# Performance work log

Hardware: AMD Instinct MI355X
Metric: run time of the kernel (lower is better)

The kernel has to match this reference:

```python
import jax, jax.numpy as jnp
import numpy as np

TEMPERATURE = 0.5   # cfg.LOSS.TEMPERATURE
REG = 0.5           # Sinkhorn entropic regularization
NUM_ITER = 100      # numItermax in forward call
STOP_THR = 1e-9

BS, NUM_CLASSES, DIM = 16384, 1000, 512


def _l2norm(x):
    return x / jnp.linalg.norm(x, axis=-1, keepdims=True)


def setup_inputs() -> dict:
    key = jax.random.key(0)
    k1, k2, k3 = jax.random.split(key, 3)
    features = _l2norm(jax.random.normal(k1, (BS, DIM), jnp.float32))
    text_features = _l2norm(jax.random.normal(k2, (NUM_CLASSES, DIM), jnp.float32))
    ratios = jax.random.uniform(k3, (NUM_CLASSES,), jnp.float32)
    ratios = ratios / ratios.sum()  # class prior, sums to 1
    return {"features": features, "text_features": text_features, "ratios": ratios}


def sinkhorn_knopp(a, b, M, reg):
    """Faithful Sinkhorn-Knopp: u/v scaling loop with NaN/Inf bail-out and
    every-10-iters convergence check, unrolled as a masked lax.scan."""
    dim_a, dim_b = a.shape[0], b.shape[0]
    K = jnp.exp(M / -reg)                 # [dim_a, dim_b]
    Kp = (1.0 / a)[:, None] * K           # [dim_a, dim_b]
    u0 = jnp.ones((dim_a,), M.dtype) / dim_a
    v0 = jnp.ones((dim_b,), M.dtype) / dim_b

    def step(carry, ii):
        u, v, done = carry
        KtU = K.T @ u                     # [dim_b]
        v_new = b / KtU
        u_new = 1.0 / (Kp @ v_new)        # [dim_a]
        bad = (jnp.any(KtU == 0)
               | jnp.any(~jnp.isfinite(u_new))
               | jnp.any(~jnp.isfinite(v_new)))
        # err check (original does it when ii % 10 == 0)
        tmp2 = (u_new @ K) * v_new        # einsum('i,ij,j->j', u, K, v)
        err = jnp.linalg.norm(tmp2 - b)
        converged = ((ii % 10) == 0) & (err < STOP_THR)
        keep_prev = done | bad            # revert to uprev/vprev on bad, freeze after done
        u2 = jnp.where(keep_prev, u, u_new)
        v2 = jnp.where(keep_prev, v, v_new)
        return (u2, v2, done | bad | converged), None

    (u, v, _), _ = jax.lax.scan(step, (u0, v0, jnp.array(False)), jnp.arange(NUM_ITER))
    return u[:, None] * K * v[None, :]


def reference(features, text_features, ratios):
    sim_matrix = (features @ text_features.T) / TEMPERATURE   # [bs, C]
    cost_matrix = 1.0 - sim_matrix
    bs = features.shape[0]
    a = jnp.ones((bs,), features.dtype)       # row marginal (uniform over batch)
    b = ratios * bs                            # column marginal (class ratios)
    plan = sinkhorn_knopp(a, b, sim_matrix / cost_matrix, REG)  # [bs, C]
    return plan
```

## Files before the change

### kernel.cpp

```cpp
#include <hip/hip_runtime.h>
#include <hip/hip_bf16.h>

typedef float   f32x4_t  __attribute__((ext_vector_type(4)));
typedef __bf16  bf16x8_t __attribute__((ext_vector_type(8)));
typedef int     i32x4_t  __attribute__((ext_vector_type(4)));

#define N_ROWS   16384
#define N_COLS   1000
#define N_COLS_P 1024
#define N_DIM    512
#define N_ITER   100
#define FUSE_BLOCKS 512
#define R12_BLOCKS  16

__device__ __forceinline__ unsigned short f2bf(float f) {
    unsigned int u = __builtin_bit_cast(unsigned int, f);
    u += 0x7FFFu + ((u >> 16) & 1u);
    return (unsigned short)(u >> 16);
}

template <int MODE>
__launch_bounds__(256)
__global__ void k_gemm(const float* __restrict__ F, const float* __restrict__ T,
                       void* __restrict__ Kout, float* __restrict__ cpart,
                       const float* __restrict__ v_com, const float* __restrict__ u_both,
                       const int* __restrict__ flags)
{
    __shared__ unsigned short lA[128 * 72];
    __shared__ unsigned short lB[128 * 72];
    __shared__ float cs_lds[4 * 64];

    const int bm = blockIdx.x;
    const int bn = blockIdx.y;
    const int m0 = bm << 7;
    const int n0 = bn << 7;
    const int t  = threadIdx.x;
    const int lane = t & 63;
    const int wid  = t >> 6;
    const int wr = wid >> 1;
    const int wc = wid & 1;

    f32x4_t acc[4][4];
#pragma unroll
    for (int a = 0; a < 4; ++a)
#pragma unroll
        for (int b = 0; b < 4; ++b)
            acc[a][b] = (f32x4_t){0.f, 0.f, 0.f, 0.f};

    const int srow = t >> 4;
    const int scol = (t & 15) << 2;

    for (int kt = 0; kt < N_DIM; kt += 64) {
#pragma unroll
        for (int r = 0; r < 8; ++r) {
            const int rr = srow + (r << 4);
            const float4 av = *(const float4*)(F + (size_t)(m0 + rr) * N_DIM + kt + scol);
            ushort4 a4; a4.x = f2bf(av.x); a4.y = f2bf(av.y); a4.z = f2bf(av.z); a4.w = f2bf(av.w);
            *(ushort4*)(&lA[rr * 72 + scol]) = a4;
            const int gn = n0 + rr;
            float4 bv = make_float4(0.f, 0.f, 0.f, 0.f);
            if (gn < N_COLS) bv = *(const float4*)(T + (size_t)gn * N_DIM + kt + scol);
            ushort4 b4; b4.x = f2bf(bv.x); b4.y = f2bf(bv.y); b4.z = f2bf(bv.z); b4.w = f2bf(bv.w);
            *(ushort4*)(&lB[rr * 72 + scol]) = b4;
        }
        __syncthreads();
#pragma unroll
        for (int ks = 0; ks < 2; ++ks) {
            bf16x8_t afr[4], bfr[4];
#pragma unroll
            for (int mf = 0; mf < 4; ++mf) {
                const int r = (wr << 6) + (mf << 4) + (lane & 15);
                const int off = r * 72 + (ks << 5) + ((lane >> 4) << 3);
                afr[mf] = __builtin_bit_cast(bf16x8_t, *(const i32x4_t*)(&lA[off]));
            }
#pragma unroll
            for (int nf = 0; nf < 4; ++nf) {
                const int r = (wc << 6) + (nf << 4) + (lane & 15);
                const int off = r * 72 + (ks << 5) + ((lane >> 4) << 3);
                bfr[nf] = __builtin_bit_cast(bf16x8_t, *(const i32x4_t*)(&lB[off]));
            }
#pragma unroll
            for (int mf = 0; mf < 4; ++mf)
#pragma unroll
                for (int nf = 0; nf < 4; ++nf)
                    acc[mf][nf] = __builtin_amdgcn_mfma_f32_16x16x32_bf16(
                        afr[mf], bfr[nf], acc[mf][nf], 0, 0, 0);
        }
        __syncthreads();
    }

    int usel = 2;
    if (MODE == 1) usel = flags[1];
    float csum[4] = {0.f, 0.f, 0.f, 0.f};
#pragma unroll
    for (int mf = 0; mf < 4; ++mf) {
#pragma unroll
        for (int nf = 0; nf < 4; ++nf) {
#pragma unroll
            for (int j = 0; j < 4; ++j) {
                const float d = acc[mf][nf][j];
                const float s = 2.f * d;
                const float M = s / (1.f - s);
                const float kv = __expf(-2.f * M);
                const int grow = m0 + (wr << 6) + (mf << 4) + ((lane >> 4) << 2) + j;
                const int gcol = n0 + (wc << 6) + (nf << 4) + (lane & 15);
                if (MODE == 0) {
                    ((unsigned short*)Kout)[(size_t)grow * N_COLS_P + gcol] =
                        (gcol < N_COLS) ? f2bf(kv) : (unsigned short)0;
                    csum[nf] += kv;
                } else {
                    if (gcol < N_COLS) {
                        const float u = (usel == 2) ? (1.f / 16384.f)
                                                    : u_both[(size_t)usel * N_ROWS + grow];
                        ((float*)Kout)[(size_t)grow * N_COLS + gcol] = u * kv * v_com[gcol];
                    }
                }
            }
        }
    }
    if (MODE == 0) {
#pragma unroll
        for (int nf = 0; nf < 4; ++nf) {
            csum[nf] += __shfl_xor(csum[nf], 16);
            csum[nf] += __shfl_xor(csum[nf], 32);
        }
        if (lane < 16) {
#pragma unroll
            for (int nf = 0; nf < 4; ++nf)
                cs_lds[wid * 64 + (nf << 4) + lane] = csum[nf];
        }
        __syncthreads();
        if (t < 128) {
            const int cw = t >> 6;
            const int c6 = t & 63;
            cpart[(size_t)bm * N_COLS_P + n0 + t] =
                cs_lds[cw * 64 + c6] + cs_lds[(cw + 2) * 64 + c6];
        }
    }
}

__launch_bounds__(128)
__global__ void k_init(const float* __restrict__ cpart, float* __restrict__ KtU0,
                       float* __restrict__ v_com, float* __restrict__ err2slots,
                       int* __restrict__ flags)
{
    const int j = blockIdx.x * 128 + threadIdx.x;
    if (j < N_COLS) {
        float s = 0.f;
        for (int p = 0; p < 128; ++p) s += cpart[(size_t)p * N_COLS_P + j];
        KtU0[j] = s * (1.f / 16384.f);
        v_com[j] = 1.f / 1000.f;
    }
    if (blockIdx.x == 0 && threadIdx.x == 0) {
        flags[0] = 0; flags[1] = 2; flags[2] = 0; flags[3] = 0;
    }
    if (blockIdx.x == 0 && threadIdx.x < R12_BLOCKS) err2slots[threadIdx.x] = 0.f;
}

__launch_bounds__(256)
__global__ void k_fuse(const unsigned short* __restrict__ Kb, const float* __restrict__ ratios,
                       const float* __restrict__ KtU_cur, float* __restrict__ u_out,
                       float* __restrict__ partials, int* __restrict__ flags)
{
    if (*(volatile int*)&flags[0]) return;
    __shared__ float vnew[N_COLS_P];
    __shared__ float wp[4][N_COLS_P];
    const int t = threadIdx.x;
    const int lane = t & 63;
    const int wid  = t >> 6;
    for (int j = t; j < N_COLS_P; j += 256) {
        float v = 0.f;
        if (j < N_COLS) v = (ratios[j] * 16384.f) / KtU_cur[j];
        vnew[j] = v;
    }
    __syncthreads();

    const int c0 = lane << 4;
    float vr[16];
#pragma unroll
    for (int e = 0; e < 16; ++e) vr[e] = vnew[c0 + e];
    float creg[16];
#pragma unroll
    for (int e = 0; e < 16; ++e) creg[e] = 0.f;

    const int base_row = blockIdx.x * 32 + wid * 8;
    const unsigned short* rowp = Kb + (size_t)base_row * N_COLS_P + c0;
#pragma unroll
    for (int r = 0; r < 8; ++r) {
        const i32x4_t d0 = *(const i32x4_t*)(rowp);
        const i32x4_t d1 = *(const i32x4_t*)(rowp + 8);
        rowp += N_COLS_P;
        float kv[16];
#pragma unroll
        for (int q = 0; q < 4; ++q) {
            kv[2*q]     = __builtin_bit_cast(float, (unsigned)d0[q] << 16);
            kv[2*q+1]   = __builtin_bit_cast(float, (unsigned)d0[q] & 0xFFFF0000u);
            kv[8+2*q]   = __builtin_bit_cast(float, (unsigned)d1[q] << 16);
            kv[8+2*q+1] = __builtin_bit_cast(float, (unsigned)d1[q] & 0xFFFF0000u);
        }
        float p0 = kv[0]*vr[0], p1 = kv[1]*vr[1], p2 = kv[2]*vr[2], p3 = kv[3]*vr[3];
#pragma unroll
        for (int e = 4; e < 16; e += 4) {
            p0 += kv[e]*vr[e]; p1 += kv[e+1]*vr[e+1];
            p2 += kv[e+2]*vr[e+2]; p3 += kv[e+3]*vr[e+3];
        }
        float dot = (p0 + p1) + (p2 + p3);
#pragma unroll
        for (int s = 32; s; s >>= 1) dot += __shfl_xor(dot, s);
        const float u = 1.f / dot;
        if (lane == 0) {
            u_out[base_row + r] = u;
            if (!isfinite(u)) atomicOr(&flags[2], 1);
        }
#pragma unroll
        for (int e = 0; e < 16; ++e) creg[e] += kv[e] * u;
    }
#pragma unroll
    for (int q = 0; q < 4; ++q)
        *(float4*)(&wp[wid][c0 + (q << 2)]) =
            make_float4(creg[4*q], creg[4*q+1], creg[4*q+2], creg[4*q+3]);
    __syncthreads();
    {
        const int j4 = t << 2;
        const float4 A = *(const float4*)(&wp[0][j4]);
        const float4 B = *(const float4*)(&wp[1][j4]);
        const float4 C = *(const float4*)(&wp[2][j4]);
        const float4 D = *(const float4*)(&wp[3][j4]);
        *(float4*)(&partials[(size_t)blockIdx.x * N_COLS_P + j4]) =
            make_float4(A.x+B.x+C.x+D.x, A.y+B.y+C.y+D.y,
                        A.z+B.z+C.z+D.z, A.w+B.w+C.w+D.w);
    }
}

__launch_bounds__(256)
__global__ void k_r12(const float* __restrict__ partials, const float* __restrict__ KtU_cur,
                      float* __restrict__ KtU_next, const float* __restrict__ ratios,
                      float* __restrict__ v_com, float* __restrict__ err2slots,
                      int* __restrict__ flags, int ii, int parity)
{
    if (*(volatile int*)&flags[0]) return;
    const int t = threadIdx.x;
    const int jl = t & 63;
    const int q  = t >> 6;
    const int j  = blockIdx.x * 64 + jl;
    float s = 0.f;
    const float* pp = partials + (size_t)(q * 128) * N_COLS_P + j;
#pragma unroll 8
    for (int p = 0; p < 128; ++p) { s += *pp; pp += N_COLS_P; }
    __shared__ float red[4][64];
    __shared__ int s_last;
    red[q][jl] = s;
    __syncthreads();
    if (t < 64) {
        const int jj = blockIdx.x * 64 + t;
        float errc = 0.f;
        if (jj < N_COLS) {
            const float sum = red[0][t] + red[1][t] + red[2][t] + red[3][t];
            KtU_next[jj] = sum;
            const float b  = ratios[jj] * 16384.f;
            const float kc = KtU_cur[jj];
            const float vn = b / kc;
            if (kc == 0.f || !isfinite(vn)) atomicOr(&flags[2], 1);
            const float d = sum * vn - b;
            errc = d * d;
        }
#pragma unroll
        for (int sh = 32; sh; sh >>= 1) errc += __shfl_xor(errc, sh);
        if (t == 0) {
            err2slots[blockIdx.x] = errc;
            __threadfence();
            s_last = (atomicAdd(&flags[3], 1) == R12_BLOCKS - 1) ? 1 : 0;
        }
    }
    __syncthreads();
    if (s_last) {
        __threadfence();
        const int bad = *(volatile int*)&flags[2];
        if (!bad) {
            for (int jj = t; jj < N_COLS; jj += 256)
                v_com[jj] = (ratios[jj] * 16384.f) / KtU_cur[jj];
        }
        if (t == 0) {
            float e2 = 0.f;
            for (int b2 = 0; b2 < R12_BLOCKS; ++b2) e2 += err2slots[b2];
            flags[3] = 0;
            if (bad) { flags[0] = 1; flags[2] = 0; }
            else {
                flags[1] = parity;
                if ((ii % 10) == 0 && e2 < 1e-18f) flags[0] = 1;
            }
        }
    }
}

extern "C" void kernel_launch(void* const* d_in, const int* in_sizes, int n_in,
                              void* d_out, int out_size, void* d_ws, size_t ws_size,
                              hipStream_t stream)
{
    const float* F      = (const float*)d_in[0];
    const float* T      = (const float*)d_in[1];
    const float* ratios = (const float*)d_in[2];
    float* out = (float*)d_out;
    unsigned short* Kb = (unsigned short*)d_out;

    float* ws        = (float*)d_ws;
    float* partials  = ws;
    float* ktu       = partials + (size_t)FUSE_BLOCKS * N_COLS_P;
    float* utmp      = ktu + 2 * N_COLS_P;
    float* vcom      = utmp + 2 * N_ROWS;
    float* err2slots = vcom + N_COLS_P;
    int*   flags     = (int*)(err2slots + R12_BLOCKS);
    const size_t need_bytes = ((size_t)FUSE_BLOCKS * N_COLS_P + 2 * N_COLS_P +
                               2 * N_ROWS + N_COLS_P + R12_BLOCKS) * sizeof(float)
                              + 4 * sizeof(int);
    if (ws_size < need_bytes) return;

    k_gemm<0><<<dim3(128, 8), 256, 0, stream>>>(F, T, Kb, partials, nullptr, nullptr, flags);
    k_init<<<8, 128, 0, stream>>>(partials, ktu, vcom, err2slots, flags);
    for (int ii = 0; ii < N_ITER; ++ii) {
        const int p = ii & 1;
        k_fuse<<<FUSE_BLOCKS, 256, 0, stream>>>(Kb, ratios, ktu + p * N_COLS_P,
                                                utmp + (size_t)p * N_ROWS, partials, flags);
        k_r12<<<R12_BLOCKS, 256, 0, stream>>>(partials, ktu + p * N_COLS_P,
                                              ktu + (1 - p) * N_COLS_P, ratios, vcom,
                                              err2slots, flags, ii, p);
    }
    k_gemm<1><<<dim3(128, 8), 256, 0, stream>>>(F, T, out, nullptr, vcom, utmp, flags);
}
```

Before: 2.222 ms.

## Replace per-iteration kernel pair with persistent kernel using grid barriers

Replaces the 200 per-iteration launches (fuse + reduce) with a single persistent kernel of 256 blocks that holds its slice of the bf16 K matrix in registers across all Sinkhorn iterations. Iterations are separated by hand-written atomic grid barriers, and the column reduction and error check are spread across all blocks. This aims to remove launch overhead and re-reading of K from memory each iteration. The cost is two grid barriers per iteration and a dependence on all 256 blocks being co-resident, which deadlocks if they are not.

```diff
diff --git a/kernel.cpp b/kernel.cpp
--- a/kernel.cpp
+++ b/kernel.cpp
@@ -2,6 +2,7 @@
 #include <hip/hip_bf16.h>
 
 typedef float   f32x4_t  __attribute__((ext_vector_type(4)));
+typedef float   f32x2_t  __attribute__((ext_vector_type(2)));
 typedef __bf16  bf16x8_t __attribute__((ext_vector_type(8)));
 typedef int     i32x4_t  __attribute__((ext_vector_type(4)));
 
@@ -10,13 +11,53 @@
 #define N_COLS_P 1024
 #define N_DIM    512
 #define N_ITER   100
-#define FUSE_BLOCKS 512
-#define R12_BLOCKS  16
+#define PBLK     256
+#define PTHR     512
 
 __device__ __forceinline__ unsigned short f2bf(float f) {
     unsigned int u = __builtin_bit_cast(unsigned int, f);
     u += 0x7FFFu + ((u >> 16) & 1u);
     return (unsigned short)(u >> 16);
+}
+
+__device__ __forceinline__ void unpack16(const i32x4_t a, const i32x4_t b, float kv[16]) {
+#pragma unroll
+    for (int q = 0; q < 4; ++q) {
+        kv[2*q]     = __builtin_bit_cast(float, ((unsigned)a[q]) << 16);
+        kv[2*q+1]   = __builtin_bit_cast(float, ((unsigned)a[q]) & 0xFFFF0000u);
+        kv[8+2*q]   = __builtin_bit_cast(float, ((unsigned)b[q]) << 16);
+        kv[8+2*q+1] = __builtin_bit_cast(float, ((unsigned)b[q]) & 0xFFFF0000u);
+    }
+}
+
+__device__ __forceinline__ void gridbar(int* bar, int g) {
+    __syncthreads();
+    if (blockIdx.x == 0) {
+        if (threadIdx.x == 0)
+            __hip_atomic_store(bar + 0, g, __ATOMIC_RELEASE, __HIP_MEMORY_SCOPE_AGENT);
+        if (threadIdx.x < 64) {
+            const int l = threadIdx.x;
+            for (;;) {
+                int ok = 1;
+#pragma unroll
+                for (int h = 0; h < 4; ++h)
+                    ok &= (__hip_atomic_load(bar + (h << 6) + l, __ATOMIC_RELAXED,
+                                             __HIP_MEMORY_SCOPE_AGENT) >= g);
+                if (__all(ok)) break;
+                __builtin_amdgcn_s_sleep(1);
+            }
+            __threadfence();
+            if (l == 0)
+                __hip_atomic_store(bar + 256, g, __ATOMIC_RELEASE, __HIP_MEMORY_SCOPE_AGENT);
+        }
+    } else {
+        if (threadIdx.x == 0) {
+            __hip_atomic_store(bar + blockIdx.x, g, __ATOMIC_RELEASE, __HIP_MEMORY_SCOPE_AGENT);
+            while (__hip_atomic_load(bar + 256, __ATOMIC_ACQUIRE, __HIP_MEMORY_SCOPE_AGENT) < g)
+                __builtin_amdgcn_s_sleep(2);
+        }
+    }
+    __syncthreads();
 }
 
 template <int MODE>
@@ -140,157 +181,176 @@
 }
 
 __launch_bounds__(128)
-__global__ void k_init(const float* __restrict__ cpart, float* __restrict__ KtU0,
-                       float* __restrict__ v_com, float* __restrict__ err2slots,
-                       int* __restrict__ flags)
+__global__ void k_init(const float* __restrict__ cpart, float* __restrict__ ktu0,
+                       float* __restrict__ vcom, float* __restrict__ err2,
+                       int* __restrict__ flags, int* __restrict__ bar)
 {
     const int j = blockIdx.x * 128 + threadIdx.x;
     if (j < N_COLS) {
         float s = 0.f;
         for (int p = 0; p < 128; ++p) s += cpart[(size_t)p * N_COLS_P + j];
-        KtU0[j] = s * (1.f / 16384.f);
-        v_com[j] = 1.f / 1000.f;
-    }
-    if (blockIdx.x == 0 && threadIdx.x == 0) {
-        flags[0] = 0; flags[1] = 2; flags[2] = 0; flags[3] = 0;
-    }
-    if (blockIdx.x == 0 && threadIdx.x < R12_BLOCKS) err2slots[threadIdx.x] = 0.f;
-}
-
-__launch_bounds__(256)
-__global__ void k_fuse(const unsigned short* __restrict__ Kb, const float* __restrict__ ratios,
-                       const float* __restrict__ KtU_cur, float* __restrict__ u_out,
-                       float* __restrict__ partials, int* __restrict__ flags)
+        ktu0[j] = s * (1.f / 16384.f);
+        vcom[j] = 1.f / 1000.f;
+    } else {
+        ktu0[j] = 1.f;
+        vcom[j] = 0.f;
+    }
+    if (j < 256) { err2[j] = 0.f; bar[j] = 0; }
+    if (j == 257) bar[256] = 0;
+    if (j == 0) { flags[0] = 0; flags[1] = 2; flags[2] = 0; flags[3] = 0; }
+}
+
+__launch_bounds__(PTHR, 2)
+__global__ void k_persist(const unsigned short* __restrict__ Kb,
+                          const float* __restrict__ ratios,
+                          float* __restrict__ ktu,
+                          float* __restrict__ utmp,
+                          float* __restrict__ vcom,
+                          float* __restrict__ partials,
+                          float* __restrict__ err2,
+                          int* __restrict__ flags,
+                          int* __restrict__ bar)
 {
-    if (*(volatile int*)&flags[0]) return;
-    __shared__ float vnew[N_COLS_P];
-    __shared__ float wp[4][N_COLS_P];
-    const int t = threadIdx.x;
-    const int lane = t & 63;
-    const int wid  = t >> 6;
-    for (int j = t; j < N_COLS_P; j += 256) {
-        float v = 0.f;
-        if (j < N_COLS) v = (ratios[j] * 16384.f) / KtU_cur[j];
-        vnew[j] = v;
-    }
-    __syncthreads();
-
+    __shared__ float wp[8][N_COLS_P];
+    __shared__ float errw[4];
+    __shared__ int ibc[2];
+    const int t = threadIdx.x, lane = t & 63, wid = t >> 6, b = blockIdx.x;
     const int c0 = lane << 4;
-    float vr[16];
-#pragma unroll
-    for (int e = 0; e < 16; ++e) vr[e] = vnew[c0 + e];
-    float creg[16];
-#pragma unroll
-    for (int e = 0; e < 16; ++e) creg[e] = 0.f;
-
-    const int base_row = blockIdx.x * 32 + wid * 8;
-    const unsigned short* rowp = Kb + (size_t)base_row * N_COLS_P + c0;
+    const int row0 = (b << 6) + (wid << 3);
+    const int jr = (b << 2) + wid;
+
+    i32x4_t ka[8], kb2[8];
 #pragma unroll
     for (int r = 0; r < 8; ++r) {
-        const i32x4_t d0 = *(const i32x4_t*)(rowp);
-        const i32x4_t d1 = *(const i32x4_t*)(rowp + 8);
-        rowp += N_COLS_P;
-        float kv[16];
+        const unsigned short* p = Kb + (size_t)(row0 + r) * N_COLS_P + c0;
+        ka[r]  = *(const i32x4_t*)p;
+        kb2[r] = *(const i32x4_t*)(p + 8);
+    }
+    float breg[16];
+#pragma unroll
+    for (int e = 0; e < 16; ++e)
+        breg[e] = (c0 + e < N_COLS) ? ratios[c0 + e] * 16384.f : 0.f;
+
+    int bar_g = 0;
+    int usel = 2;
+
+    for (int ii = 0; ii < N_ITER; ++ii) {
+        const int p = ii & 1;
+        const float* __restrict__ ktu_cur = ktu + p * N_COLS_P;
+        float* __restrict__ ktu_nxt = ktu + (1 - p) * N_COLS_P;
+
+        float vr[16]; int badl = 0;
 #pragma unroll
         for (int q = 0; q < 4; ++q) {
-            kv[2*q]     = __builtin_bit_cast(float, (unsigned)d0[q] << 16);
-            kv[2*q+1]   = __builtin_bit_cast(float, (unsigned)d0[q] & 0xFFFF0000u);
-            kv[8+2*q]   = __builtin_bit_cast(float, (unsigned)d1[q] << 16);
-            kv[8+2*q+1] = __builtin_bit_cast(float, (unsigned)d1[q] & 0xFFFF0000u);
-        }
-        float p0 = kv[0]*vr[0], p1 = kv[1]*vr[1], p2 = kv[2]*vr[2], p3 = kv[3]*vr[3];
-#pragma unroll
-        for (int e = 4; e < 16; e += 4) {
-            p0 += kv[e]*vr[e]; p1 += kv[e+1]*vr[e+1];
-            p2 += kv[e+2]*vr[e+2]; p3 += kv[e+3]*vr[e+3];
-        }
-        float dot = (p0 + p1) + (p2 + p3);
-#pragma unroll
-        for (int s = 32; s; s >>= 1) dot += __shfl_xor(dot, s);
-        const float u = 1.f / dot;
+            const f32x4_t k4 = *(const f32x4_t*)(ktu_cur + c0 + (q << 2));
+#pragma unroll
+            for (int e = 0; e < 4; ++e) {
+                const float v = breg[(q << 2) + e] / k4[e];
+                vr[(q << 2) + e] = v;
+                badl |= !isfinite(v);
+            }
+        }
+        float dots[8];
+#pragma unroll
+        for (int r = 0; r < 8; ++r) {
+            float kv[16];
+            unpack16(ka[r], kb2[r], kv);
+            float p0 = kv[0]*vr[0], p1 = kv[1]*vr[1], p2 = kv[2]*vr[2], p3 = kv[3]*vr[3];
+#pragma unroll
+            for (int e = 4; e < 16; e += 4) {
+                p0 = fmaf(kv[e],   vr[e],   p0); p1 = fmaf(kv[e+1], vr[e+1], p1);
+                p2 = fmaf(kv[e+2], vr[e+2], p2); p3 = fmaf(kv[e+3], vr[e+3], p3);
+            }
+            dots[r] = (p0 + p1) + (p2 + p3);
+        }
+#pragma unroll
+        for (int s = 1; s <= 32; s <<= 1) {
+#pragma unroll
+            for (int r = 0; r < 8; ++r) dots[r] += __shfl_xor(dots[r], s);
+        }
+        float u8[8];
+#pragma unroll
+        for (int r = 0; r < 8; ++r) { u8[r] = 1.f / dots[r]; badl |= !isfinite(u8[r]); }
         if (lane == 0) {
-            u_out[base_row + r] = u;
-            if (!isfinite(u)) atomicOr(&flags[2], 1);
-        }
-#pragma unroll
-        for (int e = 0; e < 16; ++e) creg[e] += kv[e] * u;
-    }
-#pragma unroll
-    for (int q = 0; q < 4; ++q)
-        *(float4*)(&wp[wid][c0 + (q << 2)]) =
-            make_float4(creg[4*q], creg[4*q+1], creg[4*q+2], creg[4*q+3]);
-    __syncthreads();
-    {
-        const int j4 = t << 2;
-        const float4 A = *(const float4*)(&wp[0][j4]);
-        const float4 B = *(const float4*)(&wp[1][j4]);
-        const float4 C = *(const float4*)(&wp[2][j4]);
-        const float4 D = *(const float4*)(&wp[3][j4]);
-        *(float4*)(&partials[(size_t)blockIdx.x * N_COLS_P + j4]) =
-            make_float4(A.x+B.x+C.x+D.x, A.y+B.y+C.y+D.y,
-                        A.z+B.z+C.z+D.z, A.w+B.w+C.w+D.w);
-    }
-}
-
-__launch_bounds__(256)
-__global__ void k_r12(const float* __restrict__ partials, const float* __restrict__ KtU_cur,
-                      float* __restrict__ KtU_next, const float* __restrict__ ratios,
-                      float* __restrict__ v_com, float* __restrict__ err2slots,
-                      int* __restrict__ flags, int ii, int parity)
-{
-    if (*(volatile int*)&flags[0]) return;
-    const int t = threadIdx.x;
-    const int jl = t & 63;
-    const int q  = t >> 6;
-    const int j  = blockIdx.x * 64 + jl;
-    float s = 0.f;
-    const float* pp = partials + (size_t)(q * 128) * N_COLS_P + j;
-#pragma unroll 8
-    for (int p = 0; p < 128; ++p) { s += *pp; pp += N_COLS_P; }
-    __shared__ float red[4][64];
-    __shared__ int s_last;
-    red[q][jl] = s;
-    __syncthreads();
-    if (t < 64) {
-        const int jj = blockIdx.x * 64 + t;
-        float errc = 0.f;
-        if (jj < N_COLS) {
-            const float sum = red[0][t] + red[1][t] + red[2][t] + red[3][t];
-            KtU_next[jj] = sum;
-            const float b  = ratios[jj] * 16384.f;
-            const float kc = KtU_cur[jj];
-            const float vn = b / kc;
-            if (kc == 0.f || !isfinite(vn)) atomicOr(&flags[2], 1);
-            const float d = sum * vn - b;
-            errc = d * d;
-        }
-#pragma unroll
-        for (int sh = 32; sh; sh >>= 1) errc += __shfl_xor(errc, sh);
-        if (t == 0) {
-            err2slots[blockIdx.x] = errc;
-            __threadfence();
-            s_last = (atomicAdd(&flags[3], 1) == R12_BLOCKS - 1) ? 1 : 0;
-        }
-    }
-    __syncthreads();
-    if (s_last) {
-        __threadfence();
-        const int bad = *(volatile int*)&flags[2];
-        if (!bad) {
-            for (int jj = t; jj < N_COLS; jj += 256)
-                v_com[jj] = (ratios[jj] * 16384.f) / KtU_cur[jj];
-        }
-        if (t == 0) {
-            float e2 = 0.f;
-            for (int b2 = 0; b2 < R12_BLOCKS; ++b2) e2 += err2slots[b2];
-            flags[3] = 0;
-            if (bad) { flags[0] = 1; flags[2] = 0; }
-            else {
-                flags[1] = parity;
-                if ((ii % 10) == 0 && e2 < 1e-18f) flags[0] = 1;
-            }
-        }
-    }
+            float* uo = utmp + (size_t)p * N_ROWS + row0;
+#pragma unroll
+            for (int r = 0; r < 8; ++r) uo[r] = u8[r];
+        }
+        if (__any(badl) && lane == 0) atomicOr(&flags[2], 1);
+
+        float creg[16];
+#pragma unroll
+        for (int e = 0; e < 16; ++e) creg[e] = 0.f;
+#pragma unroll
+        for (int r = 0; r < 8; ++r) {
+            float kv[16];
+            unpack16(ka[r], kb2[r], kv);
+#pragma unroll
+            for (int e = 0; e < 16; ++e) creg[e] = fmaf(kv[e], u8[r], creg[e]);
+        }
+#pragma unroll
+        for (int q = 0; q < 4; ++q)
+            *(f32x4_t*)&wp[wid][c0 + (q << 2)] =
+                (f32x4_t){creg[(q<<2)], creg[(q<<2)+1], creg[(q<<2)+2], creg[(q<<2)+3]};
+        __syncthreads();
+        {
+            const int j2 = t << 1;
+            f32x2_t s2 = *(const f32x2_t*)&wp[0][j2];
+#pragma unroll
+            for (int w = 1; w < 8; ++w) {
+                const f32x2_t x = *(const f32x2_t*)&wp[w][j2];
+                s2[0] += x[0]; s2[1] += x[1];
+            }
+            *(f32x2_t*)&partials[(size_t)b * N_COLS_P + j2] = s2;
+        }
+        ++bar_g; gridbar(bar, bar_g);
+
+        if (t == 0) ibc[0] = __hip_atomic_load(&flags[2], __ATOMIC_RELAXED,
+                                               __HIP_MEMORY_SCOPE_AGENT);
+        __syncthreads();
+        const int bad = ibc[0];
+        if (!bad && wid < 4) {
+            float s = 0.f;
+#pragma unroll
+            for (int h = 0; h < 4; ++h)
+                s += partials[(size_t)((h << 6) + lane) * N_COLS_P + jr];
+#pragma unroll
+            for (int sh = 1; sh <= 32; sh <<= 1) s += __shfl_xor(s, sh);
+            if (lane == 0) {
+                float errc = 0.f;
+                if (jr < N_COLS) {
+                    ktu_nxt[jr] = s;
+                    const float bj = ratios[jr] * 16384.f;
+                    const float vn = bj / ktu_cur[jr];
+                    const float d  = s * vn - bj;
+                    errc = d * d;
+                } else {
+                    ktu_nxt[jr] = 1.f;
+                }
+                errw[wid] = errc;
+            }
+        }
+        __syncthreads();
+        if (!bad && t == 0) err2[b] = (errw[0] + errw[1]) + (errw[2] + errw[3]);
+        ++bar_g; gridbar(bar, bar_g);
+
+        if (bad) break;
+        usel = p;
+        if ((ii % 10) == 0) {
+            float e = (t < 256) ? err2[t] : 0.f;
+#pragma unroll
+            for (int sh = 1; sh <= 32; sh <<= 1) e += __shfl_xor(e, sh);
+            if (t < 256 && lane == 0) errw[wid] = e;
+            __syncthreads();
+            if (t == 0) ibc[1] = ((errw[0] + errw[1] + errw[2] + errw[3]) < 1e-18f) ? 1 : 0;
+            __syncthreads();
+            if (ibc[1]) break;
+        }
+    }
+
+    if (wid < 4 && lane == 0 && usel != 2 && jr < N_COLS)
+        vcom[jr] = (ratios[jr] * 16384.f) / ktu[(size_t)usel * N_COLS_P + jr];
+    if (b == 0 && t == 0) flags[1] = usel;
 }
 
 extern "C" void kernel_launch(void* const* d_in, const int* in_sizes, int n_in,
@@ -305,25 +365,19 @@
 
     float* ws        = (float*)d_ws;
     float* partials  = ws;
-    float* ktu       = partials + (size_t)FUSE_BLOCKS * N_COLS_P;
+    float* ktu       = partials + (size_t)PBLK * N_COLS_P;
     float* utmp      = ktu + 2 * N_COLS_P;
     float* vcom      = utmp + 2 * N_ROWS;
-    float* err2slots = vcom + N_COLS_P;
-    int*   flags     = (int*)(err2slots + R12_BLOCKS);
-    const size_t need_bytes = ((size_t)FUSE_BLOCKS * N_COLS_P + 2 * N_COLS_P +
-                               2 * N_ROWS + N_COLS_P + R12_BLOCKS) * sizeof(float)
-                              + 4 * sizeof(int);
+    float* err2      = vcom + N_COLS_P;
+    int*   flags     = (int*)(err2 + 256);
+    int*   bar       = flags + 4;
+    const size_t need_bytes = ((size_t)PBLK * N_COLS_P + 2 * N_COLS_P + 2 * N_ROWS +
+                               N_COLS_P + 256) * sizeof(float) + (4 + 257) * sizeof(int);
     if (ws_size < need_bytes) return;
 
     k_gemm<0><<<dim3(128, 8), 256, 0, stream>>>(F, T, Kb, partials, nullptr, nullptr, flags);
-    k_init<<<8, 128, 0, stream>>>(partials, ktu, vcom, err2slots, flags);
-    for (int ii = 0; ii < N_ITER; ++ii) {
-        const int p = ii & 1;
-        k_fuse<<<FUSE_BLOCKS, 256, 0, stream>>>(Kb, ratios, ktu + p * N_COLS_P,
-                                                utmp + (size_t)p * N_ROWS, partials, flags);
-        k_r12<<<R12_BLOCKS, 256, 0, stream>>>(partials, ktu + p * N_COLS_P,
-                                              ktu + (1 - p) * N_COLS_P, ratios, vcom,
-                                              err2slots, flags, ii, p);
-    }
+    k_init<<<8, 128, 0, stream>>>(partials, ktu, vcom, err2, flags, bar);
+    k_persist<<<PBLK, PTHR, 0, stream>>>(Kb, ratios, ktu, utmp, vcom, partials,
+                                         err2, flags, bar);
     k_gemm<1><<<dim3(128, 8), 256, 0, stream>>>(F, T, out, nullptr, vcom, utmp, flags);
 }
```

Result: slower. 4.808 ms (+116.4%).
